# Optimization experiments

Hardware: AMD Instinct MI355X
Metric: run time of the kernel (lower is better)

## Reference

```python
import jax, jax.numpy as jnp
import numpy as np

B, NUM_TAGS, SEQ_LEN, HIDDEN = 8, 1024, 4096, 256
BLOCK = SEQ_LEN // NUM_TAGS  # tokens per tag block


def setup_inputs() -> dict:
    key = jax.random.key(0)
    k1, k2 = jax.random.split(key)
    inputs = jax.random.normal(k1, (B, SEQ_LEN, HIDDEN), dtype=jnp.float32)
    # Structured tag->token mask: tag i covers token block i and (overlapping) block i+1,
    # mimicking nested HTML tags; the suffix-subtraction in the module resolves overlaps.
    tag_idx = jnp.arange(NUM_TAGS)[:, None]           # [T,1]
    tok_blk = jnp.arange(SEQ_LEN)[None, :] // BLOCK   # [1,S]
    mask = ((tok_blk == tag_idx) | (tok_blk == tag_idx + 1)).astype(jnp.float32)
    tag_to_token = jnp.broadcast_to(mask, (B, NUM_TAGS, SEQ_LEN))
    seq_emb = jax.random.normal(k2, (NUM_TAGS, HIDDEN), dtype=jnp.float32) * 0.02
    return {"inputs": inputs, "tag_to_token": tag_to_token, "seq_emb": seq_emb}


def _deduce_direct_string(tag_to_token):
    # Binary indicator of positive entries
    binm = (tag_to_token > 0).astype(tag_to_token.dtype)          # [B,T,S]
    # Exclusive suffix sum over the tag axis (rows below i), replacing the Python loop
    suffix_incl = jnp.flip(jnp.cumsum(jnp.flip(binm, axis=1), axis=1), axis=1)
    temp = binm - (suffix_incl - binm)                            # bin[i] - sum_{j>i} bin[j]
    temp = jnp.maximum(temp, 0.0)                                 # temp[temp<=0]=0
    # Row-normalize over tokens; empty rows divide by 1
    s = jnp.sum(temp, axis=2, keepdims=True)
    return temp / jnp.where(s == 0, 1.0, s)


def reference(inputs, tag_to_token, seq_emb):
    modified = _deduce_direct_string(tag_to_token)                # [B,T,S]
    out = jnp.einsum('bts,bsh->bth', modified, inputs)            # [B,T,H]
    num_tags = out.shape[1]
    return out + seq_emb[None, :num_tags, :]
```

## Files before the change

### kernel.cpp

```cpp
#include <hip/hip_runtime.h>

#define B_ 8
#define T_ 1024
#define S_ 4096
#define H_ 256

#define STRIP 64
#define CHUNK 128

__global__ void __launch_bounds__(256) colmax_pipe_kernel(const float* __restrict__ ttt,
                                                          int* __restrict__ L) {
    __shared__ unsigned long long wmask[2][4];
    __shared__ int red[4][STRIP];
    const int strippos = blockIdx.x >> 3;
    const int b  = blockIdx.x & 7;
    const int s0 = strippos * STRIP;
    const int w    = threadIdx.x >> 6;
    const int lane = threadIdx.x & 63;

    const float* colbase = ttt + (size_t)b * T_ * S_ + s0 + lane;

    int best = -1;
    int par = 0;
    float v[32], vn[32];

    {
        const float* p = colbase + (size_t)(T_ - CHUNK + w * 32) * S_;
#pragma unroll
        for (int j = 0; j < 32; ++j)
            v[j] = p[(size_t)j * S_];
    }

    for (int thi = T_; thi > 0; thi -= CHUNK) {
        const int t0 = thi - CHUNK + w * 32;
        if (thi > CHUNK) {
            const float* pn = colbase + (size_t)(t0 - CHUNK) * S_;
#pragma unroll
            for (int j = 0; j < 32; ++j)
                vn[j] = pn[(size_t)j * S_];
        }
        int lm = -1;
#pragma unroll
        for (int j = 0; j < 32; ++j)
            if (v[j] > 0.0f) lm = t0 + j;
        best = max(best, lm);

        wmask[par][w] = __ballot(best >= 0);
        __syncthreads();
        unsigned long long all = wmask[par][0] | wmask[par][1]
                               | wmask[par][2] | wmask[par][3];
        if (all == ~0ull) break;
        par ^= 1;
#pragma unroll
        for (int j = 0; j < 32; ++j)
            v[j] = vn[j];
    }

    red[w][lane] = best;
    __syncthreads();
    if (threadIdx.x < STRIP) {
        int m = max(max(red[0][threadIdx.x], red[1][threadIdx.x]),
                    max(red[2][threadIdx.x], red[3][threadIdx.x]));
        L[b * S_ + s0 + threadIdx.x] = m;
    }
}

__global__ void gather_mean_kernel(const float* __restrict__ inputs,
                                   const int* __restrict__ L,
                                   const float* __restrict__ seq_emb,
                                   float* __restrict__ out) {
    int wid  = threadIdx.x >> 6;
    int lane = threadIdx.x & 63;
    int bt = blockIdx.x * 4 + wid;
    int b = bt >> 10;
    int t = bt & (T_ - 1);

    const int4* Lb4 = reinterpret_cast<const int4*>(L + b * S_);
    const float4* in4 = reinterpret_cast<const float4*>(inputs);

    float4 acc = {0.0f, 0.0f, 0.0f, 0.0f};
    int c = 0;

#pragma unroll 4
    for (int c0 = 0; c0 < S_ / 4; c0 += 64) {
        int4 v = Lb4[c0 + lane];
        unsigned long long m0 = __ballot(v.x == t);
        unsigned long long m1 = __ballot(v.y == t);
        unsigned long long m2 = __ballot(v.z == t);
        unsigned long long m3 = __ballot(v.w == t);
        while (m0) { int l = __ffsll(m0) - 1; m0 &= m0 - 1;
            int s = (c0 + l) * 4 + 0;
            float4 r = in4[(size_t)(b * S_ + s) * (H_ / 4) + lane];
            acc.x += r.x; acc.y += r.y; acc.z += r.z; acc.w += r.w; c++; }
        while (m1) { int l = __ffsll(m1) - 1; m1 &= m1 - 1;
            int s = (c0 + l) * 4 + 1;
            float4 r = in4[(size_t)(b * S_ + s) * (H_ / 4) + lane];
            acc.x += r.x; acc.y += r.y; acc.z += r.z; acc.w += r.w; c++; }
        while (m2) { int l = __ffsll(m2) - 1; m2 &= m2 - 1;
            int s = (c0 + l) * 4 + 2;
            float4 r = in4[(size_t)(b * S_ + s) * (H_ / 4) + lane];
            acc.x += r.x; acc.y += r.y; acc.z += r.z; acc.w += r.w; c++; }
        while (m3) { int l = __ffsll(m3) - 1; m3 &= m3 - 1;
            int s = (c0 + l) * 4 + 3;
            float4 r = in4[(size_t)(b * S_ + s) * (H_ / 4) + lane];
            acc.x += r.x; acc.y += r.y; acc.z += r.z; acc.w += r.w; c++; }
    }

    float inv = (c > 0) ? (1.0f / (float)c) : 0.0f;
    float4 e = reinterpret_cast<const float4*>(seq_emb)[t * (H_ / 4) + lane];
    float4 o;
    o.x = acc.x * inv + e.x;
    o.y = acc.y * inv + e.y;
    o.z = acc.z * inv + e.z;
    o.w = acc.w * inv + e.w;
    reinterpret_cast<float4*>(out)[(size_t)bt * (H_ / 4) + lane] = o;
}

extern "C" void kernel_launch(void* const* d_in, const int* in_sizes, int n_in,
                              void* d_out, int out_size, void* d_ws, size_t ws_size,
                              hipStream_t stream) {
    const float* inputs  = (const float*)d_in[0];
    const float* ttt     = (const float*)d_in[1];
    const float* seq_emb = (const float*)d_in[2];
    float* out = (float*)d_out;
    int* L = (int*)d_ws;

    colmax_pipe_kernel<<<B_ * (S_ / STRIP), 256, 0, stream>>>(ttt, L);

    gather_mean_kernel<<<B_ * T_ / 4, 256, 0, stream>>>(inputs, L, seq_emb, out);
}
```

Measured before the change: 30.07 us.

## Record per-strip tag ranges and skip strips in gather kernel

The column-max kernel now also writes, for each 64-token strip, the minimum and maximum owning tag index. The gather kernel reads these ranges with one ballot and scans only the strips whose range can contain its tag, instead of scanning all 4096 label entries per tag row. This cuts the per-wave scan of the L array from 16 iterations down to a few strips, at the cost of a small extra reduction and write in the first kernel.

```diff
diff --git a/kernel.cpp b/kernel.cpp
--- a/kernel.cpp
+++ b/kernel.cpp
@@ -9,7 +9,8 @@
 #define CHUNK 128
 
 __global__ void __launch_bounds__(256) colmax_pipe_kernel(const float* __restrict__ ttt,
-                                                          int* __restrict__ L) {
+                                                          int* __restrict__ L,
+                                                          int2* __restrict__ range) {
     __shared__ unsigned long long wmask[2][4];
     __shared__ int red[4][STRIP];
     const int strippos = blockIdx.x >> 3;
@@ -59,51 +60,53 @@
     red[w][lane] = best;
     __syncthreads();
     if (threadIdx.x < STRIP) {
-        int m = max(max(red[0][threadIdx.x], red[1][threadIdx.x]),
-                    max(red[2][threadIdx.x], red[3][threadIdx.x]));
-        L[b * S_ + s0 + threadIdx.x] = m;
+        const int tid = threadIdx.x;
+        int m = max(max(red[0][tid], red[1][tid]),
+                    max(red[2][tid], red[3][tid]));
+        L[b * S_ + s0 + tid] = m;
+        int mn = (m < 0) ? 0x7fffffff : m;
+        int mx = m;
+#pragma unroll
+        for (int k = 32; k >= 1; k >>= 1) {
+            mn = min(mn, __shfl_xor(mn, k));
+            mx = max(mx, __shfl_xor(mx, k));
+        }
+        if (tid == 0) {
+            int2 rg = {mn, mx};
+            range[b * (S_ / STRIP) + strippos] = rg;
+        }
     }
 }
 
-__global__ void gather_mean_kernel(const float* __restrict__ inputs,
-                                   const int* __restrict__ L,
-                                   const float* __restrict__ seq_emb,
-                                   float* __restrict__ out) {
-    int wid  = threadIdx.x >> 6;
-    int lane = threadIdx.x & 63;
-    int bt = blockIdx.x * 4 + wid;
-    int b = bt >> 10;
-    int t = bt & (T_ - 1);
+__global__ void __launch_bounds__(256) gather_range_kernel(const float* __restrict__ inputs,
+                                                           const int* __restrict__ L,
+                                                           const int2* __restrict__ range,
+                                                           const float* __restrict__ seq_emb,
+                                                           float* __restrict__ out) {
+    const int wid  = threadIdx.x >> 6;
+    const int lane = threadIdx.x & 63;
+    const int bt = blockIdx.x * 4 + wid;
+    const int b = bt >> 10;
+    const int t = bt & (T_ - 1);
 
-    const int4* Lb4 = reinterpret_cast<const int4*>(L + b * S_);
     const float4* in4 = reinterpret_cast<const float4*>(inputs);
+
+    int2 rg = range[b * (S_ / STRIP) + lane];
+    unsigned long long smask = __ballot(rg.x <= t && t <= rg.y);
 
     float4 acc = {0.0f, 0.0f, 0.0f, 0.0f};
     int c = 0;
 
-#pragma unroll 4
-    for (int c0 = 0; c0 < S_ / 4; c0 += 64) {
-        int4 v = Lb4[c0 + lane];
-        unsigned long long m0 = __ballot(v.x == t);
-        unsigned long long m1 = __ballot(v.y == t);
-        unsigned long long m2 = __ballot(v.z == t);
-        unsigned long long m3 = __ballot(v.w == t);
-        while (m0) { int l = __ffsll(m0) - 1; m0 &= m0 - 1;
-            int s = (c0 + l) * 4 + 0;
+    while (smask) {
+        int strip = __ffsll(smask) - 1; smask &= smask - 1;
+        int Lv = L[b * S_ + strip * STRIP + lane];
+        unsigned long long bm = __ballot(Lv == t);
+        while (bm) {
+            int l = __ffsll(bm) - 1; bm &= bm - 1;
+            int s = strip * STRIP + l;
             float4 r = in4[(size_t)(b * S_ + s) * (H_ / 4) + lane];
-            acc.x += r.x; acc.y += r.y; acc.z += r.z; acc.w += r.w; c++; }
-        while (m1) { int l = __ffsll(m1) - 1; m1 &= m1 - 1;
-            int s = (c0 + l) * 4 + 1;
-            float4 r = in4[(size_t)(b * S_ + s) * (H_ / 4) + lane];
-            acc.x += r.x; acc.y += r.y; acc.z += r.z; acc.w += r.w; c++; }
-        while (m2) { int l = __ffsll(m2) - 1; m2 &= m2 - 1;
-            int s = (c0 + l) * 4 + 2;
-            float4 r = in4[(size_t)(b * S_ + s) * (H_ / 4) + lane];
-            acc.x += r.x; acc.y += r.y; acc.z += r.z; acc.w += r.w; c++; }
-        while (m3) { int l = __ffsll(m3) - 1; m3 &= m3 - 1;
-            int s = (c0 + l) * 4 + 3;
-            float4 r = in4[(size_t)(b * S_ + s) * (H_ / 4) + lane];
-            acc.x += r.x; acc.y += r.y; acc.z += r.z; acc.w += r.w; c++; }
+            acc.x += r.x; acc.y += r.y; acc.z += r.z; acc.w += r.w; c++;
+        }
     }
 
     float inv = (c > 0) ? (1.0f / (float)c) : 0.0f;
@@ -123,9 +126,11 @@
     const float* ttt     = (const float*)d_in[1];
     const float* seq_emb = (const float*)d_in[2];
     float* out = (float*)d_out;
+
     int* L = (int*)d_ws;
+    int2* range = (int2*)(L + B_ * S_);
 
-    colmax_pipe_kernel<<<B_ * (S_ / STRIP), 256, 0, stream>>>(ttt, L);
+    colmax_pipe_kernel<<<B_ * (S_ / STRIP), 256, 0, stream>>>(ttt, L, range);
 
-    gather_mean_kernel<<<B_ * T_ / 4, 256, 0, stream>>>(inputs, L, seq_emb, out);
+    gather_range_kernel<<<B_ * T_ / 4, 256, 0, stream>>>(inputs, L, range, seq_emb, out);
 }
```

New measurement: 28.57 us (median of 3 runs). 1.05x faster.
